# Performance work log

Measured on AMD Instinct MI355X. Metric: run time of the kernel, lower is better.

Reference implementation:

```python
import jax, jax.numpy as jnp
import numpy as np
from jax import lax

DIM = 512          # input channels
H_IN = 56          # input spatial size
B = 32             # batch
C = DIM // 4       # inner attention dim = 128
WS = H_IN // 4     # window size = 14
NH = 4             # num_heads (C > 64 branch)
HD = C // NH       # head dim = 32
N = WS * WS        # tokens = 196
BN_EPS = 1e-5


def _rel_index():
    # Swin-style relative position index, matches the torch buffer computation.
    coords = np.stack(np.meshgrid(np.arange(WS), np.arange(WS), indexing='ij'))  # [2,WS,WS]
    flat = coords.reshape(2, -1)                                                 # [2,N]
    rel = (flat[:, :, None] - flat[:, None, :]).transpose(1, 2, 0).astype(np.int64)  # [N,N,2]
    rel[..., 0] += WS - 1
    rel[..., 1] += WS - 1
    rel[..., 0] *= 2 * WS - 1
    return jnp.asarray(rel.sum(-1))  # [N,N] int


def _interp_mat(n_in, scale):
    # Bilinear upsample (align_corners=True, as in nn.UpsamplingBilinear2d) as a matrix.
    n_out = n_in * scale
    src = np.arange(n_out) * (n_in - 1) / (n_out - 1)
    lo = np.floor(src).astype(np.int64)
    hi = np.minimum(lo + 1, n_in - 1)
    w = (src - lo).astype(np.float32)
    M = np.zeros((n_out, n_in), np.float32)
    M[np.arange(n_out), lo] += 1.0 - w
    M[np.arange(n_out), hi] += w
    return jnp.asarray(M)  # [n_out, n_in]


def setup_inputs() -> dict:
    key = jax.random.key(0)
    ks = jax.random.split(key, 8)
    x = jax.random.normal(ks[0], (B, DIM, H_IN, H_IN), jnp.float32)
    # grouped 4x4/stride-4 conv: groups = C, in_per_group = DIM // C = 4 -> OIHW [C,4,4,4]
    conv_w = jax.random.normal(ks[1], (C, 4, 4, 4), jnp.float32) * 0.05
    conv_b = jnp.zeros((C,), jnp.float32)
    bn_gamma = jnp.ones((C,), jnp.float32)
    bn_beta = jnp.zeros((C,), jnp.float32)
    bn_mean = jnp.zeros((C,), jnp.float32)
    bn_var = jnp.ones((C,), jnp.float32)
    qkv_w = jax.random.normal(ks[2], (3 * C, C), jnp.float32) * (C ** -0.5)
    proj_w = jax.random.normal(ks[3], (C, C), jnp.float32) * (C ** -0.5)
    proj_b = jnp.zeros((C,), jnp.float32)
    rpb_table = jax.random.normal(ks[4], ((2 * WS - 1) ** 2, NH), jnp.float32) * 0.02
    convout_w = jax.random.normal(ks[5], (DIM, C), jnp.float32) * (C ** -0.5)
    convout_b = jnp.zeros((DIM,), jnp.float32)
    return dict(x=x, conv_w=conv_w, conv_b=conv_b, bn_gamma=bn_gamma, bn_beta=bn_beta,
                bn_mean=bn_mean, bn_var=bn_var, qkv_w=qkv_w, proj_w=proj_w, proj_b=proj_b,
                rpb_table=rpb_table, convout_w=convout_w, convout_b=convout_b)


def reference(x, conv_w, conv_b, bn_gamma, bn_beta, bn_mean, bn_var,
              qkv_w, proj_w, proj_b, rpb_table, convout_w, convout_b):
    # local_embed: grouped conv 4x4 s4 -> BN (eval) -> ReLU6
    y = lax.conv_general_dilated(x, conv_w, window_strides=(4, 4), padding='VALID',
                                 dimension_numbers=('NCHW', 'OIHW', 'NCHW'),
                                 feature_group_count=C)
    y = y + conv_b[None, :, None, None]
    scale_bn = bn_gamma * lax.rsqrt(bn_var + BN_EPS)
    y = y * scale_bn[None, :, None, None] + (bn_beta - bn_mean * scale_bn)[None, :, None, None]
    y = jnp.clip(y, 0.0, 6.0)  # ReLU6

    # flatten to tokens: [B, N, C]
    t = y.reshape(B, C, N).transpose(0, 2, 1)

    # qkv projection (no bias) -> q,k,v [B, NH, N, HD]
    qkv = (t @ qkv_w.T).reshape(B, N, 3, NH, HD).transpose(2, 0, 3, 1, 4)
    q, k, v = qkv[0], qkv[1], qkv[2]
    q = q * (HD ** -0.5)

    attn = jnp.einsum('bhnd,bhmd->bhnm', q, k)  # [B,NH,N,N]
    idx = _rel_index()                           # [N,N]
    bias = rpb_table[idx.reshape(-1)].reshape(N, N, NH).transpose(2, 0, 1)  # [NH,N,N]
    attn = jax.nn.softmax(attn + bias[None], axis=-1)

    o = jnp.einsum('bhnm,bhmd->bhnd', attn, v)  # [B,NH,N,HD]
    o = o.transpose(0, 2, 1, 3).reshape(B, N, C)
    o = o @ proj_w.T + proj_b

    # blc2bchw
    o = o.reshape(B, WS, WS, C).transpose(0, 3, 1, 2)  # [B,C,WS,WS]

    # 1x1 conv back to DIM channels
    o = jnp.einsum('oc,bchw->bohw', convout_w, o) + convout_b[None, :, None, None]

    # bilinear upsample x4, align_corners=True
    M = _interp_mat(WS, 4)  # [4*WS, WS]
    o = jnp.einsum('Oh,bchw->bcOw', M, o)
    o = jnp.einsum('Pw,bchw->bchP', M, o)
    return o  # [B, DIM, H_IN, H_IN]
```

## Files before the change

### kernel.cpp

```cpp
#include <hip/hip_runtime.h>

#define QSCALE 0.17677669529663687f

__global__ __launch_bounds__(256) void conv_embed_kernel(
    const float* __restrict__ x, const float* __restrict__ cw,
    const float* __restrict__ cb, const float* __restrict__ gam,
    const float* __restrict__ bet, const float* __restrict__ mea,
    const float* __restrict__ var, float* __restrict__ tbuf)
{
  __shared__ __align__(16) float xs[12544];
  __shared__ __align__(16) float wsm[64];
  const int c = blockIdx.x, b = blockIdx.y, tid = threadIdx.x;
  const float4* xb = (const float4*)(x + (b*512 + 4*c)*3136);
  for (int t = tid; t < 3136; t += 256) ((float4*)xs)[t] = xb[t];
  if (tid < 64) wsm[tid] = cw[c*64 + tid];
  __syncthreads();
  if (tid < 196) {
    int oy = tid / 14, ox = tid - (tid/14)*14;
    float acc = cb[c];
#pragma unroll
    for (int i = 0; i < 4; ++i)
#pragma unroll
      for (int kh = 0; kh < 4; ++kh) {
        float4 xv = *(const float4*)&xs[i*3136 + (4*oy+kh)*56 + 4*ox];
        float4 wv = *(const float4*)&wsm[i*16 + kh*4];
        acc += xv.x*wv.x + xv.y*wv.y + xv.z*wv.z + xv.w*wv.w;
      }
    float sc = gam[c] * rsqrtf(var[c] + 1e-5f);
    float v = acc*sc + (bet[c] - mea[c]*sc);
    v = fminf(fmaxf(v, 0.0f), 6.0f);
    tbuf[(b*196 + tid)*128 + c] = v;
  }
}

__global__ __launch_bounds__(256) void make_wc_kernel(
    const float* __restrict__ cow, const float* __restrict__ pw,
    const float* __restrict__ pb, const float* __restrict__ cob,
    float* __restrict__ Wc, float* __restrict__ bias_c)
{
  int idx = blockIdx.x*256 + threadIdx.x;
  int oc = idx >> 7, k = idx & 127;
  float acc = 0.f;
  for (int cc = 0; cc < 128; ++cc) acc += cow[oc*128 + cc] * pw[cc*128 + k];
  Wc[idx] = acc;
  if (blockIdx.x < 2) {
    float a2 = cob[idx];
    for (int cc = 0; cc < 128; ++cc) a2 += cow[idx*128 + cc] * pb[cc];
    bias_c[idx] = a2;
  }
}

__device__ __forceinline__ void gemm_tile_64x64(
    const float* __restrict__ Ag, const float* __restrict__ Bg,
    int row0, int col0, float* As, float* Bs, float (&acc)[4][4])
{
  const int tid = threadIdx.x;
#pragma unroll
  for (int it = 0; it < 8; ++it) {
    int rr = (it & 3)*16 + (tid & 15);
    int kq = (it >> 2)*16 + (tid >> 4);
    float4 va = *(const float4*)&Ag[(row0+rr)*128 + kq*4];
    As[(4*kq+0)*68 + rr] = va.x;
    As[(4*kq+1)*68 + rr] = va.y;
    As[(4*kq+2)*68 + rr] = va.z;
    As[(4*kq+3)*68 + rr] = va.w;
    float4 vb = *(const float4*)&Bg[(col0+rr)*128 + kq*4];
    Bs[(4*kq+0)*68 + rr] = vb.x;
    Bs[(4*kq+1)*68 + rr] = vb.y;
    Bs[(4*kq+2)*68 + rr] = vb.z;
    Bs[(4*kq+3)*68 + rr] = vb.w;
  }
  __syncthreads();
  const int tx = (tid & 15)*4, ty = (tid >> 4)*4;
#pragma unroll 8
  for (int k = 0; k < 128; ++k) {
    float4 a4 = *(const float4*)&As[k*68 + ty];
    float4 b4 = *(const float4*)&Bs[k*68 + tx];
    float av[4] = {a4.x, a4.y, a4.z, a4.w};
    float bv[4] = {b4.x, b4.y, b4.z, b4.w};
#pragma unroll
    for (int i = 0; i < 4; ++i)
#pragma unroll
      for (int j = 0; j < 4; ++j) acc[i][j] += av[i]*bv[j];
  }
}

__global__ __launch_bounds__(256) void gemm_qkv_kernel(
    const float* __restrict__ t, const float* __restrict__ qkv_w,
    float* __restrict__ qkv)
{
  __shared__ __align__(16) float As[128*68];
  __shared__ __align__(16) float Bs[128*68];
  float acc[4][4] = {};
  gemm_tile_64x64(t, qkv_w, blockIdx.y*64, blockIdx.x*64, As, Bs, acc);
  const int tid = threadIdx.x;
  const int tx = (tid & 15)*4, ty = (tid >> 4)*4;
  const int col0 = blockIdx.x*64 + tx;
  const int s3 = col0 >> 7, rr = col0 & 127;
  const int hh = rr >> 5, dd = rr & 31;
  const float qs = (s3 == 0) ? QSCALE : 1.0f;
#pragma unroll
  for (int i = 0; i < 4; ++i) {
    int row = blockIdx.y*64 + ty + i;
    int bb = row / 196, nn = row - bb*196;
    float4 v;
    v.x = acc[i][0]*qs; v.y = acc[i][1]*qs; v.z = acc[i][2]*qs; v.w = acc[i][3]*qs;
    *(float4*)&qkv[(((s3*32 + bb)*4 + hh)*196 + nn)*32 + dd] = v;
  }
}

__global__ __launch_bounds__(256) void score_kernel(
    const float* __restrict__ qkv, const float* __restrict__ rpb,
    float* __restrict__ St)
{
  __shared__ __align__(16) float Ks[32*68];
  __shared__ __align__(16) float Qs[32*68];
  __shared__ float rpb_lds[729];
  const int tile = blockIdx.x, h = blockIdx.y, b = blockIdx.z;
  const int tm = (tile >> 2)*64, tn = (tile & 3)*64;
  const int tid = threadIdx.x;
  const float* qg = qkv + (b*4 + h)*6272;
  const float* kg = qkv + ((32 + b)*4 + h)*6272;
#pragma unroll
  for (int it = 0; it < 2; ++it) {
    int rr = (tid & 31) + it*32;
    int kq = tid >> 5;
    int rk = tm + rr; if (rk > 195) rk = 195;
    float4 va = *(const float4*)&kg[rk*32 + kq*4];
    Ks[(4*kq+0)*68+rr] = va.x; Ks[(4*kq+1)*68+rr] = va.y;
    Ks[(4*kq+2)*68+rr] = va.z; Ks[(4*kq+3)*68+rr] = va.w;
    int rq = tn + rr; if (rq > 195) rq = 195;
    float4 vb = *(const float4*)&qg[rq*32 + kq*4];
    Qs[(4*kq+0)*68+rr] = vb.x; Qs[(4*kq+1)*68+rr] = vb.y;
    Qs[(4*kq+2)*68+rr] = vb.z; Qs[(4*kq+3)*68+rr] = vb.w;
  }
  for (int t = tid; t < 729; t += 256) rpb_lds[t] = rpb[t*4 + h];
  __syncthreads();
  const int tx = (tid & 15)*4, ty = (tid >> 4)*4;
  float acc[4][4] = {};
#pragma unroll 8
  for (int k = 0; k < 32; ++k) {
    float4 a4 = *(const float4*)&Ks[k*68 + ty];
    float4 b4 = *(const float4*)&Qs[k*68 + tx];
    float av[4] = {a4.x, a4.y, a4.z, a4.w};
    float bv[4] = {b4.x, b4.y, b4.z, b4.w};
#pragma unroll
    for (int i = 0; i < 4; ++i)
#pragma unroll
      for (int j = 0; j < 4; ++j) acc[i][j] += av[i]*bv[j];
  }
  int ym[4], xm[4], yn[4], xn[4];
#pragma unroll
  for (int i = 0; i < 4; ++i) {
    int m = tm + ty + i; if (m > 195) m = 0;
    ym[i] = m / 14; xm[i] = m - ym[i]*14;
  }
#pragma unroll
  for (int j = 0; j < 4; ++j) {
    int n = tn + tx + j; if (n > 195) n = 0;
    yn[j] = n / 14; xn[j] = n - yn[j]*14;
  }
  float* stb = St + ((b*4 + h)*196)*200;
  const bool nfull = (tn + tx + 3 < 196);
#pragma unroll
  for (int i = 0; i < 4; ++i) {
    int m = tm + ty + i;
    if (m >= 196) continue;
    float sv[4];
#pragma unroll
    for (int j = 0; j < 4; ++j)
      sv[j] = acc[i][j] + rpb_lds[(yn[j]-ym[i]+13)*27 + (xn[j]-xm[i]+13)];
    if (nfull) {
      float4 v4; v4.x = sv[0]; v4.y = sv[1]; v4.z = sv[2]; v4.w = sv[3];
      *(float4*)&stb[m*200 + tn + tx] = v4;
    } else {
#pragma unroll
      for (int j = 0; j < 4; ++j)
        if (tn + tx + j < 196) stb[m*200 + tn + tx + j] = sv[j];
    }
  }
}

__global__ __launch_bounds__(64) void softmax_pv_kernel(
    const float* __restrict__ qkv, const float* __restrict__ St,
    float* __restrict__ o)
{
  __shared__ __align__(16) float v_lds[196*32];
  const int q4 = blockIdx.x, h = blockIdx.y, b = blockIdx.z;
  const int tid = threadIdx.x;
  const float4* vg = (const float4*)(qkv + ((64 + b)*4 + h)*6272);
  for (int t = tid; t < 1568; t += 64) ((float4*)v_lds)[t] = vg[t];
  __syncthreads();
  const int row = q4*49 + tid;
  const bool act = (tid < 49);
  const int rowc = act ? row : q4*49;
  const float* sp = St + ((b*4 + h)*196)*200 + rowc;
  float mx = -1e30f;
  for (int m = 0; m < 196; m += 4) {
    float s0 = sp[(m+0)*200], s1 = sp[(m+1)*200];
    float s2 = sp[(m+2)*200], s3 = sp[(m+3)*200];
    mx = fmaxf(mx, fmaxf(fmaxf(s0, s1), fmaxf(s2, s3)));
  }
  float4 oa[8];
#pragma unroll
  for (int d = 0; d < 8; ++d) oa[d] = make_float4(0.f, 0.f, 0.f, 0.f);
  float sum = 0.f;
#pragma unroll 2
  for (int m = 0; m < 196; ++m) {
    float e = __expf(sp[m*200] - mx);
    sum += e;
    const float4* vr = (const float4*)&v_lds[m*32];
#pragma unroll
    for (int d = 0; d < 8; ++d) {
      float4 v4 = vr[d];
      oa[d].x += e*v4.x; oa[d].y += e*v4.y;
      oa[d].z += e*v4.z; oa[d].w += e*v4.w;
    }
  }
  if (act) {
    float inv = 1.f / sum;
    float4* op = (float4*)&o[(b*196 + row)*128 + h*32];
#pragma unroll
    for (int d = 0; d < 8; ++d) {
      float4 v4;
      v4.x = oa[d].x*inv; v4.y = oa[d].y*inv;
      v4.z = oa[d].z*inv; v4.w = oa[d].w*inv;
      op[d] = v4;
    }
  }
}

__global__ __launch_bounds__(256) void gemm_out_kernel(
    const float* __restrict__ obuf, const float* __restrict__ Wc,
    const float* __restrict__ bias_c, float* __restrict__ co)
{
  __shared__ __align__(16) float As[128*68];
  __shared__ __align__(16) float Bs[128*68];
  float acc[4][4] = {};
  gemm_tile_64x64(obuf, Wc, blockIdx.y*64, blockIdx.x*64, As, Bs, acc);
  const int tid = threadIdx.x;
  const int tx = (tid & 15)*4, ty = (tid >> 4)*4;
  const int row0 = blockIdx.y*64 + ty;
  const int bb = row0 / 196, nn0 = row0 - bb*196;
#pragma unroll
  for (int j = 0; j < 4; ++j) {
    int col = blockIdx.x*64 + tx + j;
    float bc = bias_c[col];
    float4 v;
    v.x = acc[0][j] + bc; v.y = acc[1][j] + bc;
    v.z = acc[2][j] + bc; v.w = acc[3][j] + bc;
    *(float4*)&co[(bb*512 + col)*196 + nn0] = v;
  }
}

__global__ __launch_bounds__(256) void upsample_kernel(
    const float* __restrict__ co, float* __restrict__ out)
{
  __shared__ float cs[1568];
  __shared__ int lo_s[56];
  __shared__ float w_s[56];
  const int cg = blockIdx.x, b = blockIdx.y, tid = threadIdx.x;
  const float* cbase = co + (b*512 + cg*8)*196;
  for (int t = tid; t < 1568; t += 256) cs[t] = cbase[t];
  if (tid < 56) {
    double s = (double)(tid*13) / 55.0;
    int lo = (int)s;
    lo_s[tid] = lo;
    w_s[tid] = (float)(s - lo);
  }
  __syncthreads();
  float* obase = out + (b*512 + cg*8)*3136;
  for (int t4 = tid; t4 < 6272; t4 += 256) {
    int ch = t4 / 784;
    int rem = t4 - ch*784;
    int i2 = rem / 14;
    int j4 = (rem - i2*14)*4;
    int li = lo_s[i2]; float wi = w_s[i2];
    int hi = (li+1 < 13) ? li+1 : 13;
    const float* p0 = cs + ch*196 + li*14;
    const float* p1 = cs + ch*196 + hi*14;
    float4 ov;
    float* ovp = (float*)&ov;
#pragma unroll
    for (int jj = 0; jj < 4; ++jj) {
      int j2 = j4 + jj;
      int lj = lo_s[j2]; float wj = w_s[j2];
      int hj = (lj+1 < 13) ? lj+1 : 13;
      float top = p0[lj]*(1.f-wj) + p0[hj]*wj;
      float bot = p1[lj]*(1.f-wj) + p1[hj]*wj;
      ovp[jj] = top*(1.f-wi) + bot*wi;
    }
    ((float4*)obase)[t4] = ov;
  }
}

extern "C" void kernel_launch(void* const* d_in, const int* in_sizes, int n_in,
                              void* d_out, int out_size, void* d_ws, size_t ws_size,
                              hipStream_t stream)
{
  const float* x         = (const float*)d_in[0];
  const float* conv_w    = (const float*)d_in[1];
  const float* conv_b    = (const float*)d_in[2];
  const float* bn_gamma  = (const float*)d_in[3];
  const float* bn_beta   = (const float*)d_in[4];
  const float* bn_mean   = (const float*)d_in[5];
  const float* bn_var    = (const float*)d_in[6];
  const float* qkv_w     = (const float*)d_in[7];
  const float* proj_w    = (const float*)d_in[8];
  const float* proj_b    = (const float*)d_in[9];
  const float* rpb       = (const float*)d_in[10];
  const float* convout_w = (const float*)d_in[11];
  const float* convout_b = (const float*)d_in[12];
  float* out = (float*)d_out;
  float* ws  = (float*)d_ws;

  float* tbuf   = ws;
  float* qkvb   = ws + 802816;
  float* obuf   = ws + 3211264;
  float* Wc     = ws + 4014080;
  float* bias_c = ws + 4079616;
  float* St     = ws + 4080128;
  float* co     = ws + 4080128;

  conv_embed_kernel<<<dim3(128, 32), 256, 0, stream>>>(
      x, conv_w, conv_b, bn_gamma, bn_beta, bn_mean, bn_var, tbuf);
  make_wc_kernel<<<dim3(256), 256, 0, stream>>>(
      convout_w, proj_w, proj_b, convout_b, Wc, bias_c);
  gemm_qkv_kernel<<<dim3(6, 98), 256, 0, stream>>>(tbuf, qkv_w, qkvb);
  score_kernel<<<dim3(16, 4, 32), 256, 0, stream>>>(qkvb, rpb, St);
  softmax_pv_kernel<<<dim3(4, 4, 32), 64, 0, stream>>>(qkvb, St, obuf);
  gemm_out_kernel<<<dim3(8, 98), 256, 0, stream>>>(obuf, Wc, bias_c, co);
  upsample_kernel<<<dim3(64, 32), 256, 0, stream>>>(co, out);
}
```

Measured before the change: 503.8 us.

## Fuse score and softmax-PV into one flash-style attention kernel

Result: faster. 482.0 us (-4.3%).

```diff
diff --git a/kernel.cpp b/kernel.cpp
--- a/kernel.cpp
+++ b/kernel.cpp
@@ -109,124 +109,93 @@
   }
 }
 
-__global__ __launch_bounds__(256) void score_kernel(
+__global__ __launch_bounds__(256) void attn_kernel(
     const float* __restrict__ qkv, const float* __restrict__ rpb,
-    float* __restrict__ St)
-{
-  __shared__ __align__(16) float Ks[32*68];
-  __shared__ __align__(16) float Qs[32*68];
+    float* __restrict__ o)
+{
+  __shared__ __align__(16) float k_lds[196*32];
+  __shared__ __align__(16) float v_lds[196*32];
   __shared__ float rpb_lds[729];
-  const int tile = blockIdx.x, h = blockIdx.y, b = blockIdx.z;
-  const int tm = (tile >> 2)*64, tn = (tile & 3)*64;
+  __shared__ int   off_lds[196];
+  const int qhalf = blockIdx.x, h = blockIdx.y, b = blockIdx.z;
   const int tid = threadIdx.x;
-  const float* qg = qkv + (b*4 + h)*6272;
-  const float* kg = qkv + ((32 + b)*4 + h)*6272;
-#pragma unroll
-  for (int it = 0; it < 2; ++it) {
-    int rr = (tid & 31) + it*32;
-    int kq = tid >> 5;
-    int rk = tm + rr; if (rk > 195) rk = 195;
-    float4 va = *(const float4*)&kg[rk*32 + kq*4];
-    Ks[(4*kq+0)*68+rr] = va.x; Ks[(4*kq+1)*68+rr] = va.y;
-    Ks[(4*kq+2)*68+rr] = va.z; Ks[(4*kq+3)*68+rr] = va.w;
-    int rq = tn + rr; if (rq > 195) rq = 195;
-    float4 vb = *(const float4*)&qg[rq*32 + kq*4];
-    Qs[(4*kq+0)*68+rr] = vb.x; Qs[(4*kq+1)*68+rr] = vb.y;
-    Qs[(4*kq+2)*68+rr] = vb.z; Qs[(4*kq+3)*68+rr] = vb.w;
+  const float4* kg = (const float4*)(qkv + ((32 + b)*4 + h)*6272);
+  const float4* vg = (const float4*)(qkv + ((64 + b)*4 + h)*6272);
+  for (int t = tid; t < 1568; t += 256) {
+    ((float4*)k_lds)[t] = kg[t];
+    ((float4*)v_lds)[t] = vg[t];
   }
   for (int t = tid; t < 729; t += 256) rpb_lds[t] = rpb[t*4 + h];
+  if (tid < 196) { int y = tid/14; off_lds[tid] = y*27 + (tid - y*14); }
+
+  const int r = tid >> 1, half = tid & 1;
+  const bool act = (r < 98);
+  const int n = qhalf*98 + (act ? r : 0);
+  const float4* qg = (const float4*)(qkv + ((b*4 + h)*196 + n)*32);
+  float4 qv[8];
+#pragma unroll
+  for (int d = 0; d < 8; ++d) qv[d] = qg[d];
+  const int yn = n/14, xn = n - yn*14;
+  const int basen = yn*27 + xn + 364;
   __syncthreads();
-  const int tx = (tid & 15)*4, ty = (tid >> 4)*4;
-  float acc[4][4] = {};
-#pragma unroll 8
-  for (int k = 0; k < 32; ++k) {
-    float4 a4 = *(const float4*)&Ks[k*68 + ty];
-    float4 b4 = *(const float4*)&Qs[k*68 + tx];
-    float av[4] = {a4.x, a4.y, a4.z, a4.w};
-    float bv[4] = {b4.x, b4.y, b4.z, b4.w};
-#pragma unroll
-    for (int i = 0; i < 4; ++i)
-#pragma unroll
-      for (int j = 0; j < 4; ++j) acc[i][j] += av[i]*bv[j];
-  }
-  int ym[4], xm[4], yn[4], xn[4];
-#pragma unroll
-  for (int i = 0; i < 4; ++i) {
-    int m = tm + ty + i; if (m > 195) m = 0;
-    ym[i] = m / 14; xm[i] = m - ym[i]*14;
-  }
-#pragma unroll
-  for (int j = 0; j < 4; ++j) {
-    int n = tn + tx + j; if (n > 195) n = 0;
-    yn[j] = n / 14; xn[j] = n - yn[j]*14;
-  }
-  float* stb = St + ((b*4 + h)*196)*200;
-  const bool nfull = (tn + tx + 3 < 196);
-#pragma unroll
-  for (int i = 0; i < 4; ++i) {
-    int m = tm + ty + i;
-    if (m >= 196) continue;
-    float sv[4];
-#pragma unroll
-    for (int j = 0; j < 4; ++j)
-      sv[j] = acc[i][j] + rpb_lds[(yn[j]-ym[i]+13)*27 + (xn[j]-xm[i]+13)];
-    if (nfull) {
-      float4 v4; v4.x = sv[0]; v4.y = sv[1]; v4.z = sv[2]; v4.w = sv[3];
-      *(float4*)&stb[m*200 + tn + tx] = v4;
-    } else {
-#pragma unroll
-      for (int j = 0; j < 4; ++j)
-        if (tn + tx + j < 196) stb[m*200 + tn + tx + j] = sv[j];
+
+  float mx = -1e30f, sum = 0.f;
+  float4 oa[8];
+#pragma unroll
+  for (int d = 0; d < 8; ++d) oa[d] = make_float4(0.f, 0.f, 0.f, 0.f);
+  const int m0 = half*98;
+#pragma unroll 2
+  for (int i = 0; i < 98; ++i) {
+    const int m = m0 + i;
+    const float4* kr = (const float4*)&k_lds[m*32];
+    float sx = 0.f, sy = 0.f, sz = 0.f, sw = 0.f;
+#pragma unroll
+    for (int d = 0; d < 8; ++d) {
+      float4 kv = kr[d];
+      sx += qv[d].x*kv.x; sy += qv[d].y*kv.y;
+      sz += qv[d].z*kv.z; sw += qv[d].w*kv.w;
     }
-  }
-}
-
-__global__ __launch_bounds__(64) void softmax_pv_kernel(
-    const float* __restrict__ qkv, const float* __restrict__ St,
-    float* __restrict__ o)
-{
-  __shared__ __align__(16) float v_lds[196*32];
-  const int q4 = blockIdx.x, h = blockIdx.y, b = blockIdx.z;
-  const int tid = threadIdx.x;
-  const float4* vg = (const float4*)(qkv + ((64 + b)*4 + h)*6272);
-  for (int t = tid; t < 1568; t += 64) ((float4*)v_lds)[t] = vg[t];
-  __syncthreads();
-  const int row = q4*49 + tid;
-  const bool act = (tid < 49);
-  const int rowc = act ? row : q4*49;
-  const float* sp = St + ((b*4 + h)*196)*200 + rowc;
-  float mx = -1e30f;
-  for (int m = 0; m < 196; m += 4) {
-    float s0 = sp[(m+0)*200], s1 = sp[(m+1)*200];
-    float s2 = sp[(m+2)*200], s3 = sp[(m+3)*200];
-    mx = fmaxf(mx, fmaxf(fmaxf(s0, s1), fmaxf(s2, s3)));
-  }
-  float4 oa[8];
-#pragma unroll
-  for (int d = 0; d < 8; ++d) oa[d] = make_float4(0.f, 0.f, 0.f, 0.f);
-  float sum = 0.f;
-#pragma unroll 2
-  for (int m = 0; m < 196; ++m) {
-    float e = __expf(sp[m*200] - mx);
+    float s = (sx + sy) + (sz + sw) + rpb_lds[basen - off_lds[m]];
+    if (s > mx + 4.f) {
+      float sc = __expf(mx - s);
+      sum *= sc;
+#pragma unroll
+      for (int d = 0; d < 8; ++d) {
+        oa[d].x *= sc; oa[d].y *= sc; oa[d].z *= sc; oa[d].w *= sc;
+      }
+      mx = s;
+    }
+    float e = __expf(s - mx);
     sum += e;
     const float4* vr = (const float4*)&v_lds[m*32];
 #pragma unroll
     for (int d = 0; d < 8; ++d) {
-      float4 v4 = vr[d];
-      oa[d].x += e*v4.x; oa[d].y += e*v4.y;
-      oa[d].z += e*v4.z; oa[d].w += e*v4.w;
+      float4 vv = vr[d];
+      oa[d].x += e*vv.x; oa[d].y += e*vv.y;
+      oa[d].z += e*vv.z; oa[d].w += e*vv.w;
     }
   }
-  if (act) {
-    float inv = 1.f / sum;
-    float4* op = (float4*)&o[(b*196 + row)*128 + h*32];
-#pragma unroll
-    for (int d = 0; d < 8; ++d) {
-      float4 v4;
-      v4.x = oa[d].x*inv; v4.y = oa[d].y*inv;
-      v4.z = oa[d].z*inv; v4.w = oa[d].w*inv;
-      op[d] = v4;
-    }
+  float omx  = __shfl_xor(mx, 1);
+  float osum = __shfl_xor(sum, 1);
+  float M = fmaxf(mx, omx);
+  float sa = __expf(mx - M), sb = __expf(omx - M);
+  float inv = 1.f / (sum*sa + osum*sb);
+  sa *= inv; sb *= inv;
+#pragma unroll
+  for (int d = 0; d < 8; ++d) {
+    float px = __shfl_xor(oa[d].x, 1);
+    float py = __shfl_xor(oa[d].y, 1);
+    float pz = __shfl_xor(oa[d].z, 1);
+    float pw = __shfl_xor(oa[d].w, 1);
+    oa[d].x = oa[d].x*sa + px*sb;
+    oa[d].y = oa[d].y*sa + py*sb;
+    oa[d].z = oa[d].z*sa + pz*sb;
+    oa[d].w = oa[d].w*sa + pw*sb;
+  }
+  if (act && half == 0) {
+    float4* op = (float4*)&o[(b*196 + n)*128 + h*32];
+#pragma unroll
+    for (int d = 0; d < 8; ++d) op[d] = oa[d];
   }
 }
 
@@ -319,7 +288,6 @@
   float* obuf   = ws + 3211264;
   float* Wc     = ws + 4014080;
   float* bias_c = ws + 4079616;
-  float* St     = ws + 4080128;
   float* co     = ws + 4080128;
 
   conv_embed_kernel<<<dim3(128, 32), 256, 0, stream>>>(
@@ -327,8 +295,7 @@
   make_wc_kernel<<<dim3(256), 256, 0, stream>>>(
       convout_w, proj_w, proj_b, convout_b, Wc, bias_c);
   gemm_qkv_kernel<<<dim3(6, 98), 256, 0, stream>>>(tbuf, qkv_w, qkvb);
-  score_kernel<<<dim3(16, 4, 32), 256, 0, stream>>>(qkvb, rpb, St);
-  softmax_pv_kernel<<<dim3(4, 4, 32), 64, 0, stream>>>(qkvb, St, obuf);
+  attn_kernel<<<dim3(2, 4, 32), 256, 0, stream>>>(qkvb, rpb, obuf);
   gemm_out_kernel<<<dim3(8, 98), 256, 0, stream>>>(obuf, Wc, bias_c, co);
   upsample_kernel<<<dim3(64, 32), 256, 0, stream>>>(co, out);
 }
```
